# Performance work log

Hardware: AMD Instinct MI355X
Metric: run time of the kernel (lower is better)

The kernel has to match this reference:

```python
import jax, jax.numpy as jnp
import numpy as np


def setup_inputs() -> dict:
    key = jax.random.key(0)
    k1, k2, k3, k4, k5 = jax.random.split(key, 5)
    B, S, IN, OUT, R = 4, 2048, 4096, 4096, 16
    x = jax.random.normal(k1, (B, S, IN), dtype=jnp.float32)
    weight = jax.random.normal(k2, (OUT, IN), dtype=jnp.float32) * 0.02
    bias = jax.random.normal(k3, (OUT,), dtype=jnp.float32) * 0.02
    lora_A = jax.random.normal(k4, (R, IN), dtype=jnp.float32) * 0.02
    lora_B = jax.random.normal(k5, (OUT, R), dtype=jnp.float32) * 0.02
    return {"x": x, "weight": weight, "bias": bias, "lora_A": lora_A, "lora_B": lora_B}


def reference(x, weight, bias, lora_A, lora_B):
    # HiRA (Linear path): out = x @ (W * (1 + A^T B^T)^T)^T + bias
    # prod_AB[i, o] = sum_r A[r, i] * B[o, r]; adapted_weight[o, i] = W[o, i] * (prod_AB + 1)[i, o]
    prod_AB = jnp.einsum('ri,or->io', lora_A, lora_B) + 1.0       # [in, out]
    adapted_weight = weight * prod_AB.T                            # [out, in]
    # F.linear: x @ adapted_weight^T + bias
    return jnp.einsum('bsi,oi->bso', x, adapted_weight) + bias
```

## Files before the change

### kernel.cpp

```cpp
#include <hip/hip_runtime.h>
#include <hip/hip_bf16.h>
#include <stdint.h>

#define M_DIM 8192
#define N_DIM 4096
#define K_DIM 4096
#define R_DIM 16

typedef __bf16 bf16x8 __attribute__((ext_vector_type(8)));
typedef float f32x4 __attribute__((ext_vector_type(4)));
typedef unsigned short u16x8 __attribute__((ext_vector_type(8)));

#define AS1(p) ((const __attribute__((address_space(1))) void*)(p))
#define AS3(p) ((__attribute__((address_space(3))) void*)(p))

#define BAR() do { asm volatile("" ::: "memory"); __builtin_amdgcn_s_barrier(); asm volatile("" ::: "memory"); } while (0)
#define LGKM0() asm volatile("s_waitcnt lgkmcnt(0)" ::: "memory")
#define VMCNT4() asm volatile("s_waitcnt vmcnt(4)" ::: "memory")
#define VMCNT0() asm volatile("s_waitcnt vmcnt(0)" ::: "memory")

__device__ __forceinline__ unsigned short f2bf(float f) {
  unsigned u = __builtin_bit_cast(unsigned, f);
  u += 0x7FFFu + ((u >> 16) & 1u);
  return (unsigned short)(u >> 16);
}

__global__ void __launch_bounds__(256) aw_kernel(
    const float* __restrict__ W, const float* __restrict__ lA,
    const float* __restrict__ lB, unsigned short* __restrict__ awb) {
  __shared__ float Asub[16 * 512];
  __shared__ float Bsub[32 * 16];
  const int i0 = blockIdx.x * 512;
  const int o0 = blockIdx.y * 32;
  const int tid = threadIdx.x;

  for (int idx = tid; idx < 16 * 512; idx += 256) {
    int r = idx >> 9, i = idx & 511;
    Asub[idx] = lA[r * K_DIM + i0 + i];
  }
  for (int idx = tid; idx < 32 * 16; idx += 256) {
    int o = idx >> 4, r = idx & 15;
    Bsub[idx] = lB[(o0 + o) * R_DIM + r];
  }
  __syncthreads();

  for (int idx = tid; idx < 32 * 512; idx += 256) {
    int o = idx >> 9, i = idx & 511;
    float s = 1.0f;
#pragma unroll
    for (int r = 0; r < 16; ++r) s += Asub[r * 512 + i] * Bsub[o * 16 + r];
    size_t g = (size_t)(o0 + o) * K_DIM + i0 + i;
    awb[g] = f2bf(W[g] * s);
  }
}

__global__ void __launch_bounds__(256) cvt_kernel(const float* __restrict__ x,
                                                  unsigned short* __restrict__ xb) {
  const long total = (long)M_DIM * K_DIM;
  long i = ((long)blockIdx.x * 256 + threadIdx.x) * 8;
  const long stride = (long)gridDim.x * 256 * 8;
  for (; i < total; i += stride) {
    const float4* p = (const float4*)(x + i);
    float4 f0 = p[0], f1 = p[1];
    u16x8 v;
    v[0] = f2bf(f0.x); v[1] = f2bf(f0.y); v[2] = f2bf(f0.z); v[3] = f2bf(f0.w);
    v[4] = f2bf(f1.x); v[5] = f2bf(f1.y); v[6] = f2bf(f1.z); v[7] = f2bf(f1.w);
    *(u16x8*)(xb + i) = v;
  }
}

__global__ void __launch_bounds__(512, 2) gemm_kernel(
    const unsigned short* __restrict__ Ag,
    const unsigned short* __restrict__ Bg,
    const float* __restrict__ bias,
    float* __restrict__ out) {
  __shared__ __attribute__((aligned(16))) unsigned short LDS[2 * 32768];

  const int nwg = gridDim.x;
  const int q8 = nwg >> 3;
  const int wg = blockIdx.x;
  const int swz = (wg & 7) * q8 + (wg >> 3);
  const int tiles_n = N_DIM / 256;
  const int brow = (swz / tiles_n) * 256;
  const int bcol = (swz % tiles_n) * 256;

  const int tid = threadIdx.x;
  const int lane = tid & 63;
  const int w = tid >> 6;
  const int wr = w >> 2, wc = w & 3;
  const int fr = lane & 15;
  const int kq = (lane >> 4) << 3;

  const int rr = lane >> 2;
  const int cc = ((lane & 1) << 3) | ((((lane >> 1) ^ (lane >> 5)) & 1) << 4);
  const int c_sw = ((w & 1) << 5) | cc;
  const int rbase = ((w >> 1) << 4) + rr;

  const unsigned short* srcA[2][2];
#pragma unroll
  for (int h = 0; h < 2; ++h)
#pragma unroll
    for (int q = 0; q < 2; ++q)
      srcA[h][q] = Ag + (size_t)(brow + h * 128 + q * 64 + rbase) * K_DIM + c_sw;
  const long long bdelta = (long long)(Bg - Ag) + (long long)(bcol - brow) * K_DIM;

  auto stageA = [&](int buf, int h, int kt) {
#pragma unroll
    for (int q = 0; q < 2; ++q)
      __builtin_amdgcn_global_load_lds(AS1(srcA[h][q] + (size_t)kt * 64),
          AS3(&LDS[buf * 32768 + h * 8192 + q * 4096 + w * 512]), 16, 0, 0);
  };
  auto stageB = [&](int buf, int h, int kt) {
#pragma unroll
    for (int q = 0; q < 2; ++q)
      __builtin_amdgcn_global_load_lds(AS1(srcA[h][q] + bdelta + (size_t)kt * 64),
          AS3(&LDS[buf * 32768 + 16384 + h * 8192 + q * 4096 + w * 512]), 16, 0, 0);
  };

  const int rdsw = ((fr << 6) | (kq << 1)) ^ ((fr & 8) << 2);
  auto lda = [&](int buf, int m, int kk) -> bf16x8 {
    return *(const bf16x8*)((const char*)LDS +
        (buf * 65536 + wr * 16384 + (m * 2 + kk) * 1024 + rdsw));
  };
  auto ldb = [&](int buf, int n, int kk) -> bf16x8 {
    return *(const bf16x8*)((const char*)LDS +
        (buf * 65536 + 32768 + (wc >> 1) * 16384 +
         (((wc & 1) * 4 + n) * 2 + kk) * 1024 + rdsw));
  };

  f32x4 acc[8][4] = {};
  bf16x8 a[2][4], b[2][4];

  auto load_a_group = [&](int buf, int mg) {
#pragma unroll
    for (int kk = 0; kk < 2; ++kk)
#pragma unroll
      for (int mi = 0; mi < 4; ++mi)
        a[kk][mi] = lda(buf, mg + mi, kk);
  };
  auto load_b_pair = [&](int buf, int nb) {
#pragma unroll
    for (int kk = 0; kk < 2; ++kk)
#pragma unroll
      for (int ni = 0; ni < 2; ++ni)
        b[kk][nb + ni] = ldb(buf, nb + ni, kk);
  };
  auto mma_quad = [&](int mb, int nb) {
#pragma unroll
    for (int mi = 0; mi < 4; ++mi)
#pragma unroll
      for (int ni = 0; ni < 2; ++ni)
#pragma unroll
        for (int kk = 0; kk < 2; ++kk)
          acc[mb + mi][nb + ni] = __builtin_amdgcn_mfma_f32_16x16x32_bf16(
              a[kk][mi], b[kk][nb + ni], acc[mb + mi][nb + ni], 0, 0, 0);
  };

  stageB(0, 0, 0); stageB(0, 1, 0); stageA(0, 0, 0); stageA(0, 1, 0);
  stageB(1, 0, 1); stageB(1, 1, 1);
  VMCNT4();
  BAR();

#pragma unroll 1
  for (int i = 0; i < K_DIM / 128; ++i) {
    const bool more = (i < K_DIM / 128 - 1);
    const int t_odd = 2 * i + 1, t_nx0 = 2 * i + 2, t_nx1 = 2 * i + 3;

    load_a_group(0, 0); load_b_pair(0, 0);
    stageA(1, 0, t_odd);
    BAR(); LGKM0();
    __builtin_amdgcn_s_setprio(1); mma_quad(0, 0); __builtin_amdgcn_s_setprio(0);
    BAR();
    load_b_pair(0, 2);
    stageA(1, 1, t_odd);
    BAR(); LGKM0();
    __builtin_amdgcn_s_setprio(1); mma_quad(0, 2); __builtin_amdgcn_s_setprio(0);
    BAR();
    load_a_group(0, 4);
    if (more) stageB(0, 0, t_nx0);
    BAR(); LGKM0();
    __builtin_amdgcn_s_setprio(1); mma_quad(4, 2); __builtin_amdgcn_s_setprio(0);
    BAR();
    if (more) stageB(0, 1, t_nx0);
    BAR();
    __builtin_amdgcn_s_setprio(1); mma_quad(4, 0); __builtin_amdgcn_s_setprio(0);
    if (more) { VMCNT4(); } else { VMCNT0(); }
    BAR();

    load_a_group(1, 0); load_b_pair(1, 0);
    if (more) stageA(0, 0, t_nx0);
    BAR(); LGKM0();
    __builtin_amdgcn_s_setprio(1); mma_quad(0, 0); __builtin_amdgcn_s_setprio(0);
    BAR();
    load_b_pair(1, 2);
    if (more) stageA(0, 1, t_nx0);
    BAR(); LGKM0();
    __builtin_amdgcn_s_setprio(1); mma_quad(0, 2); __builtin_amdgcn_s_setprio(0);
    BAR();
    load_a_group(1, 4);
    if (more) stageB(1, 0, t_nx1);
    BAR(); LGKM0();
    __builtin_amdgcn_s_setprio(1); mma_quad(4, 2); __builtin_amdgcn_s_setprio(0);
    BAR();
    if (more) stageB(1, 1, t_nx1);
    BAR();
    __builtin_amdgcn_s_setprio(1); mma_quad(4, 0); __builtin_amdgcn_s_setprio(0);
    if (more) { VMCNT4(); } else { VMCNT0(); }
    BAR();
  }

  const int fq = (lane >> 4) * 4;
#pragma unroll
  for (int n = 0; n < 4; ++n) {
    const int col = bcol + wc * 64 + n * 16 + fr;
    const float bb = bias[col];
#pragma unroll
    for (int m = 0; m < 8; ++m) {
      const int row = brow + wr * 128 + m * 16 + fq;
      f32x4 v = acc[m][n];
#pragma unroll
      for (int j = 0; j < 4; ++j)
        out[(size_t)(row + j) * N_DIM + col] = v[j] + bb;
    }
  }
}

extern "C" void kernel_launch(void* const* d_in, const int* in_sizes, int n_in,
                              void* d_out, int out_size, void* d_ws, size_t ws_size,
                              hipStream_t stream) {
  const float* x    = (const float*)d_in[0];
  const float* W    = (const float*)d_in[1];
  const float* bias = (const float*)d_in[2];
  const float* lA   = (const float*)d_in[3];
  const float* lB   = (const float*)d_in[4];
  float* out = (float*)d_out;

  unsigned short* xb  = (unsigned short*)d_ws;
  unsigned short* awb = xb + (size_t)M_DIM * K_DIM;

  aw_kernel<<<dim3(K_DIM / 512, N_DIM / 32), 256, 0, stream>>>(W, lA, lB, awb);
  cvt_kernel<<<2048, 256, 0, stream>>>(x, xb);
  gemm_kernel<<<(M_DIM / 256) * (N_DIM / 256), 512, 0, stream>>>(xb, awb, bias, out);
}
```

Before: 311.1 us.

## Merge prep kernels into one launch and deepen GEMM global-to-LDS prefetch

The weight-adaptation and x-to-bf16 conversion kernels are merged into a single launch, with block ranges split by role. This removes one launch and the serialization between the two prep passes. The GEMM pipeline now issues A-tile stages earlier so one more tile half is in flight, and the vmcnt wait goes from 4 to 6 outstanding loads. The aim is to hide more global latency behind MFMA work. The cost is more outstanding loads and a more delicate ordering between LDS buffer reuse and the waits.

Result: faster. 302.6 us (-2.7%).

```diff
diff --git a/kernel.cpp b/kernel.cpp
--- a/kernel.cpp
+++ b/kernel.cpp
@@ -16,7 +16,7 @@
 
 #define BAR() do { asm volatile("" ::: "memory"); __builtin_amdgcn_s_barrier(); asm volatile("" ::: "memory"); } while (0)
 #define LGKM0() asm volatile("s_waitcnt lgkmcnt(0)" ::: "memory")
-#define VMCNT4() asm volatile("s_waitcnt vmcnt(4)" ::: "memory")
+#define VMCNT6() asm volatile("s_waitcnt vmcnt(6)" ::: "memory")
 #define VMCNT0() asm volatile("s_waitcnt vmcnt(0)" ::: "memory")
 
 __device__ __forceinline__ unsigned short f2bf(float f) {
@@ -25,47 +25,47 @@
   return (unsigned short)(u >> 16);
 }
 
-__global__ void __launch_bounds__(256) aw_kernel(
-    const float* __restrict__ W, const float* __restrict__ lA,
-    const float* __restrict__ lB, unsigned short* __restrict__ awb) {
+#define CVT_BLOCKS 4096
+__global__ void __launch_bounds__(256) prep_kernel(
+    const float* __restrict__ x, const float* __restrict__ W,
+    const float* __restrict__ lA, const float* __restrict__ lB,
+    unsigned short* __restrict__ xb, unsigned short* __restrict__ awb) {
   __shared__ float Asub[16 * 512];
   __shared__ float Bsub[32 * 16];
-  const int i0 = blockIdx.x * 512;
-  const int o0 = blockIdx.y * 32;
   const int tid = threadIdx.x;
 
-  for (int idx = tid; idx < 16 * 512; idx += 256) {
-    int r = idx >> 9, i = idx & 511;
-    Asub[idx] = lA[r * K_DIM + i0 + i];
-  }
-  for (int idx = tid; idx < 32 * 16; idx += 256) {
-    int o = idx >> 4, r = idx & 15;
-    Bsub[idx] = lB[(o0 + o) * R_DIM + r];
-  }
-  __syncthreads();
-
-  for (int idx = tid; idx < 32 * 512; idx += 256) {
-    int o = idx >> 9, i = idx & 511;
-    float s = 1.0f;
-#pragma unroll
-    for (int r = 0; r < 16; ++r) s += Asub[r * 512 + i] * Bsub[o * 16 + r];
-    size_t g = (size_t)(o0 + o) * K_DIM + i0 + i;
-    awb[g] = f2bf(W[g] * s);
-  }
-}
-
-__global__ void __launch_bounds__(256) cvt_kernel(const float* __restrict__ x,
-                                                  unsigned short* __restrict__ xb) {
-  const long total = (long)M_DIM * K_DIM;
-  long i = ((long)blockIdx.x * 256 + threadIdx.x) * 8;
-  const long stride = (long)gridDim.x * 256 * 8;
-  for (; i < total; i += stride) {
-    const float4* p = (const float4*)(x + i);
-    float4 f0 = p[0], f1 = p[1];
-    u16x8 v;
-    v[0] = f2bf(f0.x); v[1] = f2bf(f0.y); v[2] = f2bf(f0.z); v[3] = f2bf(f0.w);
-    v[4] = f2bf(f1.x); v[5] = f2bf(f1.y); v[6] = f2bf(f1.z); v[7] = f2bf(f1.w);
-    *(u16x8*)(xb + i) = v;
+  if (blockIdx.x < 1024) {
+    const int i0 = (blockIdx.x & 7) * 512;
+    const int o0 = (blockIdx.x >> 3) * 32;
+    for (int idx = tid; idx < 16 * 512; idx += 256) {
+      int r = idx >> 9, i = idx & 511;
+      Asub[idx] = lA[r * K_DIM + i0 + i];
+    }
+    for (int idx = tid; idx < 32 * 16; idx += 256) {
+      int o = idx >> 4, r = idx & 15;
+      Bsub[idx] = lB[(o0 + o) * R_DIM + r];
+    }
+    __syncthreads();
+    for (int idx = tid; idx < 32 * 512; idx += 256) {
+      int o = idx >> 9, i = idx & 511;
+      float s = 1.0f;
+#pragma unroll
+      for (int r = 0; r < 16; ++r) s += Asub[r * 512 + i] * Bsub[o * 16 + r];
+      size_t g = (size_t)(o0 + o) * K_DIM + i0 + i;
+      awb[g] = f2bf(W[g] * s);
+    }
+  } else {
+    const long total = (long)M_DIM * K_DIM;
+    long i = ((long)(blockIdx.x - 1024) * 256 + tid) * 8;
+    const long stride = (long)CVT_BLOCKS * 256 * 8;
+    for (; i < total; i += stride) {
+      const float4* p = (const float4*)(x + i);
+      float4 f0 = p[0], f1 = p[1];
+      u16x8 v;
+      v[0] = f2bf(f0.x); v[1] = f2bf(f0.y); v[2] = f2bf(f0.z); v[3] = f2bf(f0.w);
+      v[4] = f2bf(f1.x); v[5] = f2bf(f1.y); v[6] = f2bf(f1.z); v[7] = f2bf(f1.w);
+      *(u16x8*)(xb + i) = v;
+    }
   }
 }
 
@@ -157,55 +157,53 @@
   };
 
   stageB(0, 0, 0); stageB(0, 1, 0); stageA(0, 0, 0); stageA(0, 1, 0);
-  stageB(1, 0, 1); stageB(1, 1, 1);
-  VMCNT4();
+  stageB(1, 0, 1); stageB(1, 1, 1); stageA(1, 0, 1);
+  VMCNT6();
   BAR();
 
 #pragma unroll 1
   for (int i = 0; i < K_DIM / 128; ++i) {
     const bool more = (i < K_DIM / 128 - 1);
-    const int t_odd = 2 * i + 1, t_nx0 = 2 * i + 2, t_nx1 = 2 * i + 3;
+    const int t_cur1 = 2 * i + 1, t_nx0 = 2 * i + 2, t_nx1 = 2 * i + 3;
 
     load_a_group(0, 0); load_b_pair(0, 0);
-    stageA(1, 0, t_odd);
+    stageA(1, 1, t_cur1);
     BAR(); LGKM0();
     __builtin_amdgcn_s_setprio(1); mma_quad(0, 0); __builtin_amdgcn_s_setprio(0);
     BAR();
     load_b_pair(0, 2);
-    stageA(1, 1, t_odd);
     BAR(); LGKM0();
     __builtin_amdgcn_s_setprio(1); mma_quad(0, 2); __builtin_amdgcn_s_setprio(0);
     BAR();
     load_a_group(0, 4);
-    if (more) stageB(0, 0, t_nx0);
+    if (more) { stageB(0, 0, t_nx0); stageB(0, 1, t_nx0); }
     BAR(); LGKM0();
     __builtin_amdgcn_s_setprio(1); mma_quad(4, 2); __builtin_amdgcn_s_setprio(0);
     BAR();
-    if (more) stageB(0, 1, t_nx0);
+    if (more) stageA(0, 0, t_nx0);
     BAR();
     __builtin_amdgcn_s_setprio(1); mma_quad(4, 0); __builtin_amdgcn_s_setprio(0);
-    if (more) { VMCNT4(); } else { VMCNT0(); }
+    if (more) { VMCNT6(); } else { VMCNT0(); }
     BAR();
 
     load_a_group(1, 0); load_b_pair(1, 0);
-    if (more) stageA(0, 0, t_nx0);
+    if (more) stageA(0, 1, t_nx0);
     BAR(); LGKM0();
     __builtin_amdgcn_s_setprio(1); mma_quad(0, 0); __builtin_amdgcn_s_setprio(0);
     BAR();
     load_b_pair(1, 2);
-    if (more) stageA(0, 1, t_nx0);
     BAR(); LGKM0();
     __builtin_amdgcn_s_setprio(1); mma_quad(0, 2); __builtin_amdgcn_s_setprio(0);
     BAR();
     load_a_group(1, 4);
-    if (more) stageB(1, 0, t_nx1);
+    if (more) { stageB(1, 0, t_nx1); stageB(1, 1, t_nx1); }
     BAR(); LGKM0();
     __builtin_amdgcn_s_setprio(1); mma_quad(4, 2); __builtin_amdgcn_s_setprio(0);
     BAR();
-    if (more) stageB(1, 1, t_nx1);
+    if (more) stageA(1, 0, t_nx1);
     BAR();
     __builtin_amdgcn_s_setprio(1); mma_quad(4, 0); __builtin_amdgcn_s_setprio(0);
-    if (more) { VMCNT4(); } else { VMCNT0(); }
+    if (more) VMCNT6();
     BAR();
   }
 
@@ -238,7 +236,6 @@
   unsigned short* xb  = (unsigned short*)d_ws;
   unsigned short* awb = xb + (size_t)M_DIM * K_DIM;
 
-  aw_kernel<<<dim3(K_DIM / 512, N_DIM / 32), 256, 0, stream>>>(W, lA, lB, awb);
-  cvt_kernel<<<2048, 256, 0, stream>>>(x, xb);
+  prep_kernel<<<1024 + CVT_BLOCKS, 256, 0, stream>>>(x, W, lA, lB, xb, awb);
   gemm_kernel<<<(M_DIM / 256) * (N_DIM / 256), 512, 0, stream>>>(xb, awb, bias, out);
 }
```
